# Optimization experiments

Measured on AMD Instinct MI355X. Metric: run time of the kernel, lower is better.

## Reference

```python
import jax, jax.numpy as jnp
import numpy as np

N = 30000; F = 16; E = 300000
HD = 256; NH = 8; C = HD // NH; L = 3
S = 256; K = 128
NH_CA = 4; HDC = HD // NH_CA


def _ln(x, g, b):
    mu = jnp.mean(x, -1, keepdims=True)
    v = jnp.mean((x - mu) ** 2, -1, keepdims=True)
    return (x - mu) / jnp.sqrt(v + 1e-5) * g + b


def setup_inputs() -> dict:
    ks = iter(jax.random.split(jax.random.key(0), 64))
    def nrm(sh, s=0.05):
        return jax.random.normal(next(ks), sh, jnp.float32) * s
    def zeros(sh):
        return jnp.zeros(sh, jnp.float32)
    def ones(sh):
        return jnp.ones(sh, jnp.float32)
    inp = {}
    inp['x'] = jax.random.normal(next(ks), (N, F), jnp.float32)
    inp['edge_index'] = jax.random.randint(next(ks), (2, E), 0, N, jnp.int32)
    inp['batch'] = jnp.zeros((N,), jnp.int32)
    inp['sheet_node_idx'] = jax.random.randint(next(ks), (S, K), 0, N, jnp.int32)
    inp['sheet_features'] = jax.random.normal(next(ks), (S, F), jnp.float32)
    # pre_transform
    inp['pre_W'] = nrm((F, HD)); inp['pre_b'] = zeros((HD,))
    # stacked GATv2 layers (lin_l, lin_r, att, bias)
    inp['gat_Wl'] = nrm((L, HD, HD)); inp['gat_Wr'] = nrm((L, HD, HD))
    inp['gat_att'] = nrm((L, NH, C)); inp['gat_b'] = zeros((L, HD))
    # geometry encoder
    inp['geo_W1'] = nrm((F, HD)); inp['geo_b1'] = zeros((HD,))
    inp['geo_g1'] = ones((HD,)); inp['geo_be1'] = zeros((HD,))
    inp['geo_W2'] = nrm((HD, HD)); inp['geo_b2'] = zeros((HD,))
    inp['geo_g2'] = ones((HD,)); inp['geo_be2'] = zeros((HD,))
    # cross attention (4 heads)
    inp['ca_Wq'] = nrm((HD, HD)); inp['ca_bq'] = zeros((HD,))
    inp['ca_Wk'] = nrm((HD, HD)); inp['ca_bk'] = zeros((HD,))
    inp['ca_Wv'] = nrm((HD, HD)); inp['ca_bv'] = zeros((HD,))
    inp['ca_Wo'] = nrm((HD, HD)); inp['ca_bo'] = zeros((HD,))
    # q_mlp
    inp['q_W1'] = nrm((2 * HD, HD)); inp['q_b1'] = zeros((HD,))
    inp['q_g1'] = ones((HD,)); inp['q_be1'] = zeros((HD,))
    inp['q_W2'] = nrm((HD, HD // 2)); inp['q_b2'] = zeros((HD // 2,))
    inp['q_g2'] = ones((HD // 2,)); inp['q_be2'] = zeros((HD // 2,))
    inp['q_W3'] = nrm((HD // 2, 1)); inp['q_b3'] = zeros((1,))
    # state_done_predictor
    inp['d_W1'] = nrm((HD, HD // 2)); inp['d_b1'] = zeros((HD // 2,))
    inp['d_g1'] = ones((HD // 2,)); inp['d_be1'] = zeros((HD // 2,))
    inp['d_W2'] = nrm((HD // 2, 1)); inp['d_b2'] = zeros((1,))
    return inp


def _fwd(x, sheet_features, pre_W, pre_b, gat_Wl, gat_Wr, gat_att, gat_b,
         geo_W1, geo_b1, geo_g1, geo_be1, geo_W2, geo_b2, geo_g2, geo_be2,
         ca_Wq, ca_bq, ca_Wk, ca_bk, ca_Wv, ca_bv, ca_Wo, ca_bo,
         q_W1, q_b1, q_g1, q_be1, q_W2, q_b2, q_g2, q_be2, q_W3, q_b3,
         d_W1, d_b1, d_g1, d_be1, d_W2, d_b2,
         edge_index, batch, sheet_node_idx):
    loops = jnp.arange(N, dtype=edge_index.dtype)  # PyG GATv2Conv add_self_loops=True
    src = jnp.concatenate([edge_index[0], loops])
    dst = jnp.concatenate([edge_index[1], loops])
    h = x @ pre_W + pre_b  # [N, HD]
    for l in range(L):
        xl = (h @ gat_Wl[l]).reshape(N, NH, C)  # source messages
        xr = (h @ gat_Wr[l]).reshape(N, NH, C)  # target
        m = jax.nn.leaky_relu(xl[src] + xr[dst], 0.2)  # [E+N, NH, C]
        e = jnp.einsum('ehc,hc->eh', m, gat_att[l])
        emax = jax.ops.segment_max(e, dst, num_segments=N)
        a = jnp.exp(e - emax[dst])
        denom = jax.ops.segment_sum(a, dst, num_segments=N)
        alpha = a / (denom[dst] + 1e-16)  # scatter softmax over incoming edges
        h = jax.ops.segment_sum(alpha[:, :, None] * xl[src], dst, num_segments=N)
        h = jax.nn.elu(h.reshape(N, HD) + gat_b[l])
    cnt = jax.ops.segment_sum(jnp.ones((N,), h.dtype), batch, num_segments=1)
    g = jax.ops.segment_sum(h, batch, num_segments=1) / cnt[:, None]  # [1, HD]
    sheet = h[sheet_node_idx].mean(axis=1)  # [S, HD] per-sheet gather+mean
    geo = jax.nn.relu(_ln(sheet_features @ geo_W1 + geo_b1, geo_g1, geo_be1))
    geo = jax.nn.relu(_ln(geo @ geo_W2 + geo_b2, geo_g2, geo_be2))
    qh = (sheet @ ca_Wq + ca_bq).reshape(S, NH_CA, HDC)
    kh = (geo @ ca_Wk + ca_bk).reshape(S, NH_CA, HDC)
    vh = (geo @ ca_Wv + ca_bv).reshape(S, NH_CA, HDC)
    att = jax.nn.softmax(jnp.einsum('qhd,khd->hqk', qh, kh) / jnp.sqrt(jnp.float32(HDC)), axis=-1)
    fused = jnp.einsum('hqk,khd->qhd', att, vh).reshape(S, HD) @ ca_Wo + ca_bo
    hq = jnp.concatenate([fused, jnp.broadcast_to(g, (S, HD))], axis=1)  # [S, 2*HD]
    hq = jax.nn.relu(_ln(hq @ q_W1 + q_b1, q_g1, q_be1))
    hq = jax.nn.relu(_ln(hq @ q_W2 + q_b2, q_g2, q_be2))
    q_values = (hq @ q_W3 + q_b3)[:, 0]  # [S]
    hd = jax.nn.relu(_ln(g @ d_W1 + d_b1, d_g1, d_be1))
    done_logit = (hd @ d_W2 + d_b2)[:, 0]  # [1]
    return q_values, done_logit


def reference(x, edge_index, batch, sheet_node_idx, sheet_features, pre_W, pre_b,
              gat_Wl, gat_Wr, gat_att, gat_b,
              geo_W1, geo_b1, geo_g1, geo_be1, geo_W2, geo_b2, geo_g2, geo_be2,
              ca_Wq, ca_bq, ca_Wk, ca_bk, ca_Wv, ca_bv, ca_Wo, ca_bo,
              q_W1, q_b1, q_g1, q_be1, q_W2, q_b2, q_g2, q_be2, q_W3, q_b3,
              d_W1, d_b1, d_g1, d_be1, d_W2, d_b2):
    return _fwd(x, sheet_features, pre_W, pre_b, gat_Wl, gat_Wr, gat_att, gat_b,
                geo_W1, geo_b1, geo_g1, geo_be1, geo_W2, geo_b2, geo_g2, geo_be2,
                ca_Wq, ca_bq, ca_Wk, ca_bk, ca_Wv, ca_bv, ca_Wo, ca_bo,
                q_W1, q_b1, q_g1, q_be1, q_W2, q_b2, q_g2, q_be2, q_W3, q_b3,
                d_W1, d_b1, d_g1, d_be1, d_W2, d_b2,
                edge_index, batch, sheet_node_idx)
```

## Files before the change

### kernel.cpp

```cpp
#include <hip/hip_runtime.h>
#include <hip/hip_bf16.h>
#include <stdint.h>

#define NN 30000
#define MPAD 30080
#define FI 16
#define EE 300000
#define ETOT (EE + NN)
#define HD 256
#define NH 8
#define CH 32
#define NL 3
#define SS 256
#define KS 128
#define NHC 4
#define HC 64
#define GSB 256
#define RPB 118
#define SCB 118

typedef _Float16 half8 __attribute__((ext_vector_type(8)));
typedef _Float16 half4v __attribute__((ext_vector_type(4)));
typedef _Float16 half2v __attribute__((ext_vector_type(2)));
typedef float f32x4 __attribute__((ext_vector_type(4)));

__device__ __forceinline__ float wsum(float v) {
#pragma unroll
  for (int d = 1; d < 64; d <<= 1) v += __shfl_xor(v, d);
  return v;
}

__device__ __forceinline__ half2v mk2(_Float16 a, _Float16 b) {
  half2v r; r[0] = a; r[1] = b; return r;
}

__device__ __forceinline__ half2v h2max(half2v a, half2v b) {
#if __has_builtin(__builtin_elementwise_max)
  return __builtin_elementwise_max(a, b);
#else
  half2v r; r[0] = a[0] > b[0] ? a[0] : b[0]; r[1] = a[1] > b[1] ? a[1] : b[1];
  return r;
#endif
}

__device__ __forceinline__ float h2dot(half2v a, half2v b, float c) {
#if __has_builtin(__builtin_amdgcn_fdot2)
  return __builtin_amdgcn_fdot2(a, b, c, false);
#else
  return c + (float)a[0] * (float)b[0] + (float)a[1] * (float)b[1];
#endif
}

__device__ __forceinline__ float ln_fast(float a, int t, int n, float* red16,
    const float* __restrict__ G, const float* __restrict__ Be, bool relu)
{
  float av = (t < n) ? a : 0.f;
  float s = wsum(av), s2 = wsum(av * av);
  if ((t & 63) == 0) { red16[t >> 6] = s; red16[8 + (t >> 6)] = s2; }
  __syncthreads();
  float sum = red16[0] + red16[1] + red16[2] + red16[3];
  float sq  = red16[8] + red16[9] + red16[10] + red16[11];
  float mu = sum / n;
  float var = sq / n - mu * mu;
  float o = 0.f;
  if (t < n) {
    o = (a - mu) * rsqrtf(var + 1e-5f) * G[t] + Be[t];
    if (relu) o = fmaxf(o, 0.f);
  }
  __syncthreads();
  return o;
}

__global__ __launch_bounds__(256) void k_init(int* __restrict__ cnt,
    int* __restrict__ gcnt, _Float16* __restrict__ h16pad, int* __restrict__ csr_pad)
{
  int i = blockIdx.x * 256 + threadIdx.x;
  if (i < NN) cnt[i] = 0;
  if (i == 0) gcnt[0] = 0;
  if (i < 8) csr_pad[i] = 0;
  if (i < (MPAD - NN) * HD) h16pad[i] = (_Float16)0.f;
}

__global__ __launch_bounds__(256) void k_wconvAll(
    const float* __restrict__ Wl, const float* __restrict__ Wr,
    const float* __restrict__ geo_W2, const float* __restrict__ ca_Wq,
    const float* __restrict__ ca_Wk, const float* __restrict__ ca_Wv,
    const float* __restrict__ ca_Wo, const float* __restrict__ q_W1,
    const float* __restrict__ q_W2,
    _Float16* __restrict__ WT,
    _Float16* __restrict__ Tgeo2, _Float16* __restrict__ Tq,
    _Float16* __restrict__ Tk, _Float16* __restrict__ Tv,
    _Float16* __restrict__ To, _Float16* __restrict__ Tq1,
    _Float16* __restrict__ Tq2)
{
  int b = blockIdx.x, t = threadIdx.x;
  if (b < 1536) {
    int m = b >> 8;
    int n = b & 255;
    int l = m >> 1;
    const float* W = (m & 1) ? (Wr + (size_t)l * HD * HD) : (Wl + (size_t)l * HD * HD);
    WT[((size_t)m * HD + n) * HD + t] = (_Float16)W[t * HD + n];
    return;
  }
  b -= 1536;
  if (b < 1280) {
    int seg = b >> 8;
    int n = b & 255;
    const float* src = (seg == 0) ? geo_W2 : (seg == 1) ? ca_Wq : (seg == 2) ? ca_Wk
                     : (seg == 3) ? ca_Wv : ca_Wo;
    _Float16* dst = (seg == 0) ? Tgeo2 : (seg == 1) ? Tq : (seg == 2) ? Tk
                  : (seg == 3) ? Tv : To;
    dst[(size_t)n * 256 + t] = (_Float16)src[(size_t)t * 256 + n];
  } else if (b < 1536) {
    int n = b - 1280;
    Tq1[(size_t)n * 512 + t]       = (_Float16)q_W1[(size_t)t * 256 + n];
    Tq1[(size_t)n * 512 + 256 + t] = (_Float16)q_W1[(size_t)(256 + t) * 256 + n];
  } else {
    int n = b - 1536;
    Tq2[(size_t)n * 256 + t] = (_Float16)q_W2[(size_t)t * 128 + n];
  }
}

__global__ __launch_bounds__(256) void k_pre(const float* __restrict__ x,
    const float* __restrict__ W, const float* __restrict__ b,
    _Float16* __restrict__ H16)
{
  __shared__ float Ws[FI][HD];
  __shared__ float xs[8][FI];
  int r0 = blockIdx.x * 8;
  int t = threadIdx.x;
  for (int i = t; i < FI * HD; i += 256) Ws[i >> 8][i & 255] = W[i];
  if (t < 8 * FI) xs[t >> 4][t & 15] = x[(size_t)(r0 + (t >> 4)) * FI + (t & 15)];
  __syncthreads();
  float bj = b[t];
  for (int r = 0; r < 8; ++r) {
    float acc = bj;
#pragma unroll
    for (int k = 0; k < FI; ++k) acc += xs[r][k] * Ws[k][t];
    H16[(size_t)(r0 + r) * HD + t] = (_Float16)acc;
  }
}

__global__ __launch_bounds__(256) void k_count(const int* __restrict__ ei, int* __restrict__ cnt)
{
  int i = blockIdx.x * 256 + threadIdx.x;
  if (i >= ETOT) return;
  int dst = (i < EE) ? ei[EE + i] : (i - EE);
  atomicAdd(&cnt[dst], 1);
}

__global__ __launch_bounds__(256) void k_scanA(const int* __restrict__ cnt,
    int* __restrict__ rowptr, int* __restrict__ btot)
{
  __shared__ int wt[4];
  int b = blockIdx.x, t = threadIdx.x;
  int i = b * 256 + t;
  int v = (i < NN) ? cnt[i] : 0;
  int lane = t & 63, w = t >> 6;
  int s = v;
#pragma unroll
  for (int d = 1; d < 64; d <<= 1) {
    int u = __shfl_up(s, d);
    if (lane >= d) s += u;
  }
  if (lane == 63) wt[w] = s;
  __syncthreads();
  int off = 0;
  for (int k = 0; k < w; ++k) off += wt[k];
  if (i < NN) rowptr[i] = off + s - v;
  if (t == 255) btot[b] = off + s;
}

__global__ __launch_bounds__(128) void k_scanB(const int* __restrict__ btot,
    int* __restrict__ boff, int* __restrict__ rowptr)
{
  __shared__ int wt[2];
  int t = threadIdx.x;
  int v = (t < SCB) ? btot[t] : 0;
  int lane = t & 63, w = t >> 6;
  int s = v;
#pragma unroll
  for (int d = 1; d < 64; d <<= 1) {
    int u = __shfl_up(s, d);
    if (lane >= d) s += u;
  }
  if (lane == 63) wt[w] = s;
  __syncthreads();
  int off = (w == 1) ? wt[0] : 0;
  if (t < SCB) boff[t] = off + s - v;
  if (t == 127) rowptr[NN] = wt[0] + wt[1];
}

__global__ __launch_bounds__(256) void k_scanC(int* __restrict__ rowptr,
    const int* __restrict__ boff, int* __restrict__ wptr)
{
  int b = blockIdx.x, t = threadIdx.x;
  int i = b * 256 + t;
  if (i < NN) {
    int r = rowptr[i] + boff[b];
    rowptr[i] = r;
    wptr[i] = r;
  }
}

__global__ __launch_bounds__(256) void k_scatter(const int* __restrict__ ei,
    int* __restrict__ wptr, int* __restrict__ csr_src)
{
  int i = blockIdx.x * 256 + threadIdx.x;
  if (i >= ETOT) return;
  int src = (i < EE) ? ei[i] : (i - EE);
  int dst = (i < EE) ? ei[EE + i] : (i - EE);
  int pos = atomicAdd(&wptr[dst], 1);
  csr_src[pos] = src;
}

#define BKG 64
__global__ __launch_bounds__(512) void k_gemm16(const _Float16* __restrict__ A,
    const _Float16* __restrict__ WT,
    _Float16* __restrict__ Xl, _Float16* __restrict__ Xr)
{
  __shared__ __align__(16) _Float16 As[128 * BKG];
  __shared__ __align__(16) _Float16 Bs[256 * BKG];
  int t = threadIdx.x;
  int w = t >> 6, lane = t & 63;
  int row0 = blockIdx.x * 128;
  int ct = blockIdx.y;
  const _Float16* Bmat = WT + (size_t)ct * HD * HD;
  _Float16* Out = ct ? Xr : Xl;

  f32x4 acc[4][4] = {};
  int wr = w >> 2, wc = w & 3;

  for (int k0 = 0; k0 < HD; k0 += BKG) {
#pragma unroll
    for (int i = 0; i < 2; ++i) {
      int p = i * 512 + t;
      int row = p >> 3, s = p & 7;
      int g = s ^ (row & 7);
      __builtin_amdgcn_global_load_lds(
        (const __attribute__((address_space(1))) void*)(A + (size_t)(row0 + row) * HD + k0 + g * 8),
        (__attribute__((address_space(3))) void*)((char*)As + (i * 8 + w) * 1024),
        16, 0, 0);
    }
#pragma unroll
    for (int i = 0; i < 4; ++i) {
      int p = i * 512 + t;
      int row = p >> 3, s = p & 7;
      int g = s ^ (row & 7);
      __builtin_amdgcn_global_load_lds(
        (const __attribute__((address_space(1))) void*)(Bmat + (size_t)row * HD + k0 + g * 8),
        (__attribute__((address_space(3))) void*)((char*)Bs + (i * 8 + w) * 1024),
        16, 0, 0);
    }
    __syncthreads();
#pragma unroll
    for (int ks = 0; ks < 2; ++ks) {
      half8 af[4], bfr[4];
      int kslot = ks * 4 + (lane >> 4);
#pragma unroll
      for (int mi = 0; mi < 4; ++mi) {
        int rl = wr * 64 + mi * 16 + (lane & 15);
        int ps = kslot ^ (rl & 7);
        af[mi] = *(const half8*)((const char*)As + rl * 128 + ps * 16);
      }
#pragma unroll
      for (int ni = 0; ni < 4; ++ni) {
        int nl = wc * 64 + ni * 16 + (lane & 15);
        int ps = kslot ^ (nl & 7);
        bfr[ni] = *(const half8*)((const char*)Bs + nl * 128 + ps * 16);
      }
#pragma unroll
      for (int mi = 0; mi < 4; ++mi)
#pragma unroll
        for (int ni = 0; ni < 4; ++ni)
          acc[mi][ni] = __builtin_amdgcn_mfma_f32_16x16x32_f16(af[mi], bfr[ni], acc[mi][ni], 0, 0, 0);
    }
    __syncthreads();
  }
  int crow = (lane >> 4) * 4;
  int ccol = lane & 15;
#pragma unroll
  for (int mi = 0; mi < 4; ++mi)
#pragma unroll
    for (int ni = 0; ni < 4; ++ni) {
      size_t base_r = row0 + wr * 64 + mi * 16 + crow;
      int c = wc * 64 + ni * 16 + ccol;
#pragma unroll
      for (int r = 0; r < 4; ++r)
        Out[(base_r + r) * HD + c] = (_Float16)acc[mi][ni][r];
    }
}

__global__ __launch_bounds__(256) void k_edgeagg(const _Float16* __restrict__ Xl,
    const _Float16* __restrict__ Xr, const float* __restrict__ attw,
    const float* __restrict__ bias, const int* __restrict__ rowptr,
    const int* __restrict__ csr_src, _Float16* __restrict__ H16)
{
  int node = blockIdx.x * 4 + (threadIdx.x >> 6);
  int lane = threadIdx.x & 63;
  if (node >= NN) return;
  int st = rowptr[node], en = rowptr[node + 1];
  int n = en - st;
  int hf = lane >> 5, sl = lane & 31;
  int c = sl * 8;
  half8 xrv = *(const half8*)(Xr + (size_t)node * HD + c);
  float4 wa = *(const float4*)(attw + c);
  float4 wb = *(const float4*)(attw + c + 4);
  half2v w0 = mk2((_Float16)wa.x, (_Float16)wa.y);
  half2v w1 = mk2((_Float16)wa.z, (_Float16)wa.w);
  half2v w2 = mk2((_Float16)wb.x, (_Float16)wb.y);
  half2v w3 = mk2((_Float16)wb.z, (_Float16)wb.w);
  half2v r0 = mk2(xrv[0], xrv[1]), r1 = mk2(xrv[2], xrv[3]);
  half2v r2 = mk2(xrv[4], xrv[5]), r3 = mk2(xrv[6], xrv[7]);
  half2v c02 = mk2((_Float16)0.2f, (_Float16)0.2f);

  float mh = -1e30f, dsum = 0.f;
  half2v acch0 = {}, acch1 = {}, acch2 = {}, acch3 = {};
  int trips = (n + 1) >> 1;
  int base = st + hf;

  half8 b0 = *(const half8*)(Xl + (size_t)csr_src[base] * HD + c);
  half8 b1 = *(const half8*)(Xl + (size_t)csr_src[base + 2] * HD + c);
  half8 b2 = *(const half8*)(Xl + (size_t)csr_src[base + 4] * HD + c);

  for (int it = 0; it < trips; ++it) {
    bool valid = (2 * it + hf) < n;
    half8 xc = b0;
    b0 = b1; b1 = b2;
    {
      int nidx = csr_src[base + 2 * (it + 3)];
      b2 = *(const half8*)(Xl + (size_t)nidx * HD + c);
    }
    half2v x0 = mk2(xc[0], xc[1]), x1 = mk2(xc[2], xc[3]);
    half2v x2 = mk2(xc[4], xc[5]), x3 = mk2(xc[6], xc[7]);
    half2v s0 = x0 + r0, s1 = x1 + r1, s2 = x2 + r2, s3 = x3 + r3;
    half2v m0 = h2max(s0, s0 * c02);
    half2v m1 = h2max(s1, s1 * c02);
    half2v m2 = h2max(s2, s2 * c02);
    half2v m3 = h2max(s3, s3 * c02);
    float eA = h2dot(m1, w1, h2dot(m0, w0, 0.f));
    float eB = h2dot(m3, w3, h2dot(m2, w2, 0.f));
    float e = eA + eB;
    e += __shfl_xor(e, 1);
    e += __shfl_xor(e, 2);
    e = valid ? e : -1e30f;
    if (__any(e > mh + 4.f)) {
      float nm = fmaxf(mh, e);
      float sc = __expf(mh - nm);
      _Float16 sch16 = (_Float16)sc;
      half2v sch = mk2(sch16, sch16);
      acch0 *= sch; acch1 *= sch; acch2 *= sch; acch3 *= sch;
      dsum *= sc;
      mh = nm;
    }
    float pw = valid ? __expf(e - mh) : 0.f;
    _Float16 pwh16 = (_Float16)pw;
    half2v pwh = mk2(pwh16, pwh16);
    acch0 += pwh * x0;
    acch1 += pwh * x1;
    acch2 += pwh * x2;
    acch3 += pwh * x3;
    dsum += pw;
  }
  float a[8];
  a[0] = (float)acch0[0]; a[1] = (float)acch0[1];
  a[2] = (float)acch1[0]; a[3] = (float)acch1[1];
  a[4] = (float)acch2[0]; a[5] = (float)acch2[1];
  a[6] = (float)acch3[0]; a[7] = (float)acch3[1];
  float om = __shfl_xor(mh, 32);
  float od = __shfl_xor(dsum, 32);
  float nm = fmaxf(mh, om);
  float scs = __expf(mh - nm);
  float sco = __expf(om - nm);
  float d = dsum * scs + od * sco;
#pragma unroll
  for (int j = 0; j < 8; ++j) {
    float oa = __shfl_xor(a[j], 32);
    a[j] = a[j] * scs + oa * sco;
  }
  if (hf == 0) {
    float inv = 1.f / (d + 1e-16f);
    float4 ba = *(const float4*)(bias + c);
    float4 bb = *(const float4*)(bias + c + 4);
    float ob[8] = {ba.x, ba.y, ba.z, ba.w, bb.x, bb.y, bb.z, bb.w};
    half8 h8;
#pragma unroll
    for (int j = 0; j < 8; ++j) {
      float o = a[j] * inv + ob[j];
      o = (o > 0.f) ? o : expm1f(o);
      h8[j] = (_Float16)o;
    }
    *(half8*)(H16 + (size_t)node * HD + c) = h8;
  }
}

__global__ __launch_bounds__(256) void k_gsum(const _Float16* __restrict__ H,
    const int* __restrict__ batch, float* __restrict__ gpart, int* __restrict__ gcnt)
{
  __shared__ float flagf[RPB];
  __shared__ int scount;
  int b = blockIdx.x, t = threadIdx.x;
  int r0 = b * RPB;
  int nr = NN - r0; if (nr > RPB) nr = RPB; if (nr < 0) nr = 0;
  if (t == 0) scount = 0;
  __syncthreads();
  if (t < nr) {
    int ok = (batch[r0 + t] == 0) ? 1 : 0;
    flagf[t] = (float)ok;
    if (ok) atomicAdd(&scount, 1);
  }
  __syncthreads();
  float a0 = 0.f, a1 = 0.f, a2 = 0.f, a3 = 0.f;
  const _Float16* Hp = H + (size_t)r0 * HD + t;
  int r = 0;
  for (; r + 4 <= nr; r += 4) {
    float v0 = (float)Hp[(size_t)(r + 0) * HD];
    float v1 = (float)Hp[(size_t)(r + 1) * HD];
    float v2 = (float)Hp[(size_t)(r + 2) * HD];
    float v3 = (float)Hp[(size_t)(r + 3) * HD];
    a0 += v0 * flagf[r + 0]; a1 += v1 * flagf[r + 1];
    a2 += v2 * flagf[r + 2]; a3 += v3 * flagf[r + 3];
  }
  for (; r < nr; ++r) a0 += (float)Hp[(size_t)r * HD] * flagf[r];
  gpart[(size_t)b * HD + t] = (a0 + a1) + (a2 + a3);
  if (t == 0 && scount) atomicAdd(gcnt, scount);
}

__global__ __launch_bounds__(256) void k_tail1(const _Float16* __restrict__ h16,
    const int* __restrict__ sheet_idx, const float* __restrict__ sheet_feat,
    const float* __restrict__ geo_W1, const float* __restrict__ geo_b1,
    const float* __restrict__ geo_g1, const float* __restrict__ geo_be1,
    const float* __restrict__ gpart, const int* __restrict__ gcnt,
    float* __restrict__ gvec,
    _Float16* __restrict__ sh16, _Float16* __restrict__ g116)
{
  __shared__ float xf[FI];
  __shared__ int sidx[KS];
  __shared__ float red16[16];
  int s = blockIdx.x, t = threadIdx.x;

  if (s == SS) {
    float a0 = 0.f, a1 = 0.f, a2 = 0.f, a3 = 0.f;
    for (int b = 0; b < GSB; b += 4) {
      a0 += gpart[(size_t)b * HD + t];
      a1 += gpart[(size_t)(b + 1) * HD + t];
      a2 += gpart[(size_t)(b + 2) * HD + t];
      a3 += gpart[(size_t)(b + 3) * HD + t];
    }
    gvec[t] = ((a0 + a1) + (a2 + a3)) / (float)(*gcnt);
    return;
  }

  if (t < KS) sidx[t] = sheet_idx[s * KS + t];
  if (t >= 240) xf[t - 240] = sheet_feat[s * FI + (t - 240)];
  __syncthreads();

  float pa[8] = {};
#pragma unroll 2
  for (int r = 0; r < KS; r += 8) {
#pragma unroll
    for (int u = 0; u < 8; ++u)
      pa[u] += (float)h16[(size_t)sidx[r + u] * HD + t];
  }
  float shv = ((pa[0] + pa[1]) + (pa[2] + pa[3]) + (pa[4] + pa[5]) + (pa[6] + pa[7])) * (1.f / KS);
  sh16[(size_t)s * HD + t] = (_Float16)shv;

  float a = geo_b1[t];
#pragma unroll
  for (int k = 0; k < FI; ++k) a += xf[k] * geo_W1[k * HD + t];
  float g1 = ln_fast(a, t, 256, red16, geo_g1, geo_be1, true);
  g116[(size_t)s * HD + t] = (_Float16)g1;
}

template <int KD, int NW>
__global__ __launch_bounds__(NW * 64) void k_stageLN(
    const _Float16* __restrict__ X, const _Float16* __restrict__ WT,
    const float* __restrict__ b, const float* __restrict__ G,
    const float* __restrict__ Be, _Float16* __restrict__ Y,
    const float* __restrict__ W3, const float* __restrict__ b3,
    float* __restrict__ outq,
    const float* __restrict__ gvec,
    const float* __restrict__ dW1, const float* __restrict__ db1,
    const float* __restrict__ dg1, const float* __restrict__ dbe1,
    const float* __restrict__ dW2, const float* __restrict__ db2,
    float* __restrict__ outd)
{
  __shared__ float ps[NW * 16], ps2[NW * 16], pq[NW * 16];
  const int NCOL = NW * 64;
  int t = threadIdx.x;

  if (outd != nullptr && blockIdx.x == 16) {
    int w2 = t >> 6;
    float acc2 = db1[t];
    for (int k = 0; k < 256; ++k) acc2 += gvec[k] * dW1[(size_t)k * 128 + t];
    float s = wsum(acc2), s2v = wsum(acc2 * acc2);
    if ((t & 63) == 0) { ps[w2] = s; ps2[w2] = s2v; }
    __syncthreads();
    float S = ps[0] + ps[1], S2 = ps2[0] + ps2[1];
    float mu = S * (1.f / 128.f), var = S2 * (1.f / 128.f) - mu * mu;
    float hdv = fmaxf((acc2 - mu) * rsqrtf(var + 1e-5f) * dg1[t] + dbe1[t], 0.f);
    float o = wsum(hdv * dW2[t]);
    if ((t & 63) == 0) pq[w2] = o;
    __syncthreads();
    if (t == 0) outd[0] = pq[0] + pq[1] + db2[0];
    return;
  }

  int w = t >> 6, lane = t & 63;
  int arow = lane & 15, kg = lane >> 4;
  int m0 = blockIdx.x * 16;
  int col0 = w * 64;

  f32x4 acc[4] = {};
#pragma unroll
  for (int ks = 0; ks < KD / 32; ++ks) {
    half8 af = *(const half8*)(X + (size_t)(m0 + arow) * KD + ks * 32 + kg * 8);
#pragma unroll
    for (int n = 0; n < 4; ++n) {
      half8 bf = *(const half8*)(WT + (size_t)(col0 + n * 16 + arow) * KD + ks * 32 + kg * 8);
      acc[n] = __builtin_amdgcn_mfma_f32_16x16x32_f16(af, bf, acc[n], 0, 0, 0);
    }
  }
#pragma unroll
  for (int n = 0; n < 4; ++n) {
    float bv = b[col0 + n * 16 + arow];
#pragma unroll
    for (int r = 0; r < 4; ++r) acc[n][r] += bv;
  }
  float s[4] = {}, s2[4] = {};
#pragma unroll
  for (int n = 0; n < 4; ++n)
#pragma unroll
    for (int r = 0; r < 4; ++r) { float v = acc[n][r]; s[r] += v; s2[r] += v * v; }
#pragma unroll
  for (int d = 1; d < 16; d <<= 1)
#pragma unroll
    for (int r = 0; r < 4; ++r) { s[r] += __shfl_xor(s[r], d); s2[r] += __shfl_xor(s2[r], d); }
  if (arow == 0) {
#pragma unroll
    for (int r = 0; r < 4; ++r) {
      ps[w * 16 + kg * 4 + r] = s[r];
      ps2[w * 16 + kg * 4 + r] = s2[r];
    }
  }
  __syncthreads();
  float mu[4], rs[4];
#pragma unroll
  for (int r = 0; r < 4; ++r) {
    float S = 0.f, S2 = 0.f;
#pragma unroll
    for (int w2 = 0; w2 < NW; ++w2) { S += ps[w2 * 16 + kg * 4 + r]; S2 += ps2[w2 * 16 + kg * 4 + r]; }
    float m = S / NCOL;
    float var = S2 / NCOL - m * m;
    mu[r] = m; rs[r] = rsqrtf(var + 1e-5f);
  }
#pragma unroll
  for (int n = 0; n < 4; ++n) {
    int col = col0 + n * 16 + arow;
    float gv = G[col], bev = Be[col];
#pragma unroll
    for (int r = 0; r < 4; ++r)
      acc[n][r] = fmaxf((acc[n][r] - mu[r]) * rs[r] * gv + bev, 0.f);
  }
  if (Y) {
#pragma unroll
    for (int n = 0; n < 4; ++n) {
      int col = col0 + n * 16 + arow;
#pragma unroll
      for (int r = 0; r < 4; ++r)
        Y[(size_t)(m0 + kg * 4 + r) * NCOL + col] = (_Float16)acc[n][r];
    }
  }
  if (outq) {
    float p[4] = {};
#pragma unroll
    for (int n = 0; n < 4; ++n) {
      float w3 = W3[col0 + n * 16 + arow];
#pragma unroll
      for (int r = 0; r < 4; ++r) p[r] += acc[n][r] * w3;
    }
#pragma unroll
    for (int d = 1; d < 16; d <<= 1)
#pragma unroll
      for (int r = 0; r < 4; ++r) p[r] += __shfl_xor(p[r], d);
    if (arow == 0)
#pragma unroll
      for (int r = 0; r < 4; ++r) pq[w * 16 + kg * 4 + r] = p[r];
    __syncthreads();
    if (w == 0 && arow == 0) {
#pragma unroll
      for (int r = 0; r < 4; ++r) {
        float o = b3[0];
#pragma unroll
        for (int w2 = 0; w2 < NW; ++w2) o += pq[w2 * 16 + kg * 4 + r];
        outq[m0 + kg * 4 + r] = o;
      }
    }
  }
}

__global__ __launch_bounds__(64) void k_qkv(
    const _Float16* __restrict__ sh16, const _Float16* __restrict__ g216,
    const _Float16* __restrict__ Tq, const _Float16* __restrict__ Tk,
    const _Float16* __restrict__ Tv,
    const float* __restrict__ bq, const float* __restrict__ bk,
    const float* __restrict__ bv,
    _Float16* __restrict__ qb, _Float16* __restrict__ kb, _Float16* __restrict__ vb)
{
  int lane = threadIdx.x;
  int arow = lane & 15, kg = lane >> 4;
  int m0 = blockIdx.x * 16;
  int col0 = blockIdx.y * 64;
  int mat = blockIdx.z;
  const _Float16* X = (mat == 0) ? sh16 : g216;
  const _Float16* WT = (mat == 0) ? Tq : (mat == 1) ? Tk : Tv;
  const float* b = (mat == 0) ? bq : (mat == 1) ? bk : bv;
  _Float16* Y = (mat == 0) ? qb : (mat == 1) ? kb : vb;

  f32x4 acc[4] = {};
#pragma unroll
  for (int ks = 0; ks < 8; ++ks) {
    half8 af = *(const half8*)(X + (size_t)(m0 + arow) * 256 + ks * 32 + kg * 8);
#pragma unroll
    for (int n = 0; n < 4; ++n) {
      half8 bf = *(const half8*)(WT + (size_t)(col0 + n * 16 + arow) * 256 + ks * 32 + kg * 8);
      acc[n] = __builtin_amdgcn_mfma_f32_16x16x32_f16(af, bf, acc[n], 0, 0, 0);
    }
  }
#pragma unroll
  for (int n = 0; n < 4; ++n) {
    int col = col0 + n * 16 + arow;
    float bv2 = b[col];
#pragma unroll
    for (int r = 0; r < 4; ++r)
      Y[(size_t)(m0 + kg * 4 + r) * 256 + col] = (_Float16)(acc[n][r] + bv2);
  }
}

__global__ __launch_bounds__(64) void k_wo(
    const _Float16* __restrict__ pv16, const _Float16* __restrict__ To,
    const float* __restrict__ bo, const float* __restrict__ gvec,
    _Float16* __restrict__ hqin)
{
  int lane = threadIdx.x;
  int arow = lane & 15, kg = lane >> 4;
  int m0 = blockIdx.x * 16;
  int col0 = blockIdx.y * 64;

  f32x4 acc[4] = {};
#pragma unroll
  for (int ks = 0; ks < 8; ++ks) {
    half8 af = *(const half8*)(pv16 + (size_t)(m0 + arow) * 256 + ks * 32 + kg * 8);
#pragma unroll
    for (int n = 0; n < 4; ++n) {
      half8 bf = *(const half8*)(To + (size_t)(col0 + n * 16 + arow) * 256 + ks * 32 + kg * 8);
      acc[n] = __builtin_amdgcn_mfma_f32_16x16x32_f16(af, bf, acc[n], 0, 0, 0);
    }
  }
#pragma unroll
  for (int n = 0; n < 4; ++n) {
    int col = col0 + n * 16 + arow;
    float bv = bo[col];
    _Float16 gg = (_Float16)gvec[col];
#pragma unroll
    for (int r = 0; r < 4; ++r) {
      hqin[(size_t)(m0 + kg * 4 + r) * 512 + col] = (_Float16)(acc[n][r] + bv);
      hqin[(size_t)(m0 + kg * 4 + r) * 512 + 256 + col] = gg;
    }
  }
}

__global__ __launch_bounds__(1024) void k_attn(const _Float16* __restrict__ qb,
    const _Float16* __restrict__ kb, const _Float16* __restrict__ vb,
    _Float16* __restrict__ pv16)
{
  __shared__ float qv[HD];
  __shared__ float att[1024];
  __shared__ float red4[1024];
  __shared__ float redm[16];
  __shared__ float reds[16];
  int row = blockIdx.x, t = threadIdx.x;
  int w = t >> 6;

  if (t < 256) qv[t] = (float)qb[(size_t)row * HD + t];
  __syncthreads();

  int h = t >> 8, key = t & 255;
  float e = 0.f;
  {
    const half8* kr = (const half8*)(kb + (size_t)key * HD + h * HC);
    const float* qh = qv + h * HC;
#pragma unroll
    for (int d = 0; d < 8; ++d) {
      half8 kk = kr[d];
#pragma unroll
      for (int u = 0; u < 8; ++u) e += qh[d * 8 + u] * (float)kk[u];
    }
    e *= 0.125f;
  }
  float wm = e;
#pragma unroll
  for (int d = 1; d < 64; d <<= 1) wm = fmaxf(wm, __shfl_xor(wm, d));
  if ((t & 63) == 0) redm[w] = wm;
  __syncthreads();
  float mx = fmaxf(fmaxf(redm[4 * h], redm[4 * h + 1]), fmaxf(redm[4 * h + 2], redm[4 * h + 3]));
  float pw = __expf(e - mx);
  float ws = wsum(pw);
  if ((t & 63) == 0) reds[w] = ws;
  att[t] = pw;
  __syncthreads();

  int kq = t >> 8, j = t & 255;
  int hj = j >> 6;
  float p = 0.f;
  const float* arow = att + hj * 256 + kq * 64;
  const _Float16* vcol = vb + (size_t)(kq * 64) * HD + j;
  for (int k = 0; k < 64; ++k)
    p += arow[k] * (float)vcol[(size_t)k * HD];
  red4[t] = p;
  __syncthreads();
  if (t < 256) {
    int hh = t >> 6;
    float dsum = reds[4 * hh] + reds[4 * hh + 1] + reds[4 * hh + 2] + reds[4 * hh + 3];
    float pv = (red4[t] + red4[256 + t] + red4[512 + t] + red4[768 + t]) / dsum;
    pv16[(size_t)row * HD + t] = (_Float16)pv;
  }
}

extern "C" void kernel_launch(void* const* d_in, const int* in_sizes, int n_in,
                              void* d_out, int out_size, void* d_ws, size_t ws_size,
                              hipStream_t stream) {
  const float* x      = (const float*)d_in[0];
  const int*   ei     = (const int*)d_in[1];
  const int*   batch  = (const int*)d_in[2];
  const int*   sheet_idx = (const int*)d_in[3];
  const float* sheet_feat = (const float*)d_in[4];
  const float* pre_W  = (const float*)d_in[5];
  const float* pre_b  = (const float*)d_in[6];
  const float* gat_Wl = (const float*)d_in[7];
  const float* gat_Wr = (const float*)d_in[8];
  const float* gat_att = (const float*)d_in[9];
  const float* gat_b  = (const float*)d_in[10];
  const float* geo_W1 = (const float*)d_in[11];
  const float* geo_b1 = (const float*)d_in[12];
  const float* geo_g1 = (const float*)d_in[13];
  const float* geo_be1 = (const float*)d_in[14];
  const float* geo_W2 = (const float*)d_in[15];
  const float* geo_b2 = (const float*)d_in[16];
  const float* geo_g2 = (const float*)d_in[17];
  const float* geo_be2 = (const float*)d_in[18];
  const float* ca_Wq = (const float*)d_in[19];
  const float* ca_bq = (const float*)d_in[20];
  const float* ca_Wk = (const float*)d_in[21];
  const float* ca_bk = (const float*)d_in[22];
  const float* ca_Wv = (const float*)d_in[23];
  const float* ca_bv = (const float*)d_in[24];
  const float* ca_Wo = (const float*)d_in[25];
  const float* ca_bo = (const float*)d_in[26];
  const float* q_W1 = (const float*)d_in[27];
  const float* q_b1 = (const float*)d_in[28];
  const float* q_g1 = (const float*)d_in[29];
  const float* q_be1 = (const float*)d_in[30];
  const float* q_W2 = (const float*)d_in[31];
  const float* q_b2 = (const float*)d_in[32];
  const float* q_g2 = (const float*)d_in[33];
  const float* q_be2 = (const float*)d_in[34];
  const float* q_W3 = (const float*)d_in[35];
  const float* q_b3 = (const float*)d_in[36];
  const float* d_W1 = (const float*)d_in[37];
  const float* d_b1 = (const float*)d_in[38];
  const float* d_g1 = (const float*)d_in[39];
  const float* d_be1 = (const float*)d_in[40];
  const float* d_W2 = (const float*)d_in[41];
  const float* d_b2 = (const float*)d_in[42];

  char* wsb = (char*)d_ws;
  auto alloc = [&](size_t bytes) { char* p = wsb; wsb += (bytes + 255) & ~(size_t)255; return p; };

  _Float16* h16  = (_Float16*)alloc((size_t)MPAD * HD * 2);
  _Float16* Xl16 = (_Float16*)alloc((size_t)MPAD * HD * 2);
  _Float16* Xr16 = (_Float16*)alloc((size_t)MPAD * HD * 2);
  _Float16* WT   = (_Float16*)alloc((size_t)6 * HD * HD * 2);
  _Float16* Tgeo2 = (_Float16*)alloc((size_t)HD * HD * 2);
  _Float16* Tq   = (_Float16*)alloc((size_t)HD * HD * 2);
  _Float16* Tk   = (_Float16*)alloc((size_t)HD * HD * 2);
  _Float16* Tv   = (_Float16*)alloc((size_t)HD * HD * 2);
  _Float16* To   = (_Float16*)alloc((size_t)HD * HD * 2);
  _Float16* Tq1  = (_Float16*)alloc((size_t)HD * 512 * 2);
  _Float16* Tq2  = (_Float16*)alloc((size_t)128 * HD * 2);
  _Float16* sh16 = (_Float16*)alloc((size_t)SS * HD * 2);
  _Float16* g116 = (_Float16*)alloc((size_t)SS * HD * 2);
  _Float16* g216 = (_Float16*)alloc((size_t)SS * HD * 2);
  _Float16* qb16 = (_Float16*)alloc((size_t)SS * HD * 2);
  _Float16* kb16 = (_Float16*)alloc((size_t)SS * HD * 2);
  _Float16* vb16 = (_Float16*)alloc((size_t)SS * HD * 2);
  _Float16* pv16 = (_Float16*)alloc((size_t)SS * HD * 2);
  _Float16* hqin16 = (_Float16*)alloc((size_t)SS * 512 * 2);
  _Float16* hq116 = (_Float16*)alloc((size_t)SS * HD * 2);
  float* gpart   = (float*)alloc((size_t)GSB * HD * 4);
  float* gvec    = (float*)alloc(256 * 4);
  int* cnt       = (int*)alloc((size_t)NN * 4);
  int* rowptr    = (int*)alloc((size_t)(NN + 1) * 4);
  int* wptr      = (int*)alloc((size_t)NN * 4);
  int* csr_src   = (int*)alloc((size_t)(ETOT + 8) * 4);
  int* btot      = (int*)alloc((size_t)SCB * 4);
  int* boff      = (int*)alloc((size_t)SCB * 4);
  int* gcnt      = (int*)alloc(4);

  float* out_q = (float*)d_out;
  float* out_d = out_q + SS;

  k_init<<<118, 256, 0, stream>>>(cnt, gcnt, h16 + (size_t)NN * HD, csr_src + ETOT);

  k_count<<<(ETOT + 255) / 256, 256, 0, stream>>>(ei, cnt);
  k_scanA<<<SCB, 256, 0, stream>>>(cnt, rowptr, btot);
  k_scanB<<<1, 128, 0, stream>>>(btot, boff, rowptr);
  k_scanC<<<SCB, 256, 0, stream>>>(rowptr, boff, wptr);
  k_scatter<<<(ETOT + 255) / 256, 256, 0, stream>>>(ei, wptr, csr_src);

  k_wconvAll<<<3200, 256, 0, stream>>>(gat_Wl, gat_Wr, geo_W2, ca_Wq, ca_Wk, ca_Wv,
                                       ca_Wo, q_W1, q_W2,
                                       WT, Tgeo2, Tq, Tk, Tv, To, Tq1, Tq2);
  k_pre<<<NN / 8, 256, 0, stream>>>(x, pre_W, pre_b, h16);

  dim3 ggrid(MPAD / 128, 2);
  for (int l = 0; l < NL; ++l) {
    k_gemm16<<<ggrid, 512, 0, stream>>>(h16, WT + (size_t)l * 2 * HD * HD, Xl16, Xr16);
    k_edgeagg<<<(NN + 3) / 4, 256, 0, stream>>>(Xl16, Xr16, gat_att + l * NH * CH,
                                                gat_b + l * HD, rowptr, csr_src, h16);
  }

  k_gsum<<<GSB, 256, 0, stream>>>(h16, batch, gpart, gcnt);

  k_tail1<<<SS + 1, 256, 0, stream>>>(h16, sheet_idx, sheet_feat,
      geo_W1, geo_b1, geo_g1, geo_be1, gpart, gcnt, gvec, sh16, g116);
  k_stageLN<256, 4><<<16, 256, 0, stream>>>(g116, Tgeo2, geo_b2, geo_g2, geo_be2,
      g216, nullptr, nullptr, nullptr,
      nullptr, nullptr, nullptr, nullptr, nullptr, nullptr, nullptr, nullptr);
  dim3 qkvg(16, 4, 3);
  k_qkv<<<qkvg, 64, 0, stream>>>(sh16, g216, Tq, Tk, Tv, ca_bq, ca_bk, ca_bv,
                                 qb16, kb16, vb16);
  k_attn<<<SS, 1024, 0, stream>>>(qb16, kb16, vb16, pv16);
  dim3 wog(16, 4);
  k_wo<<<wog, 64, 0, stream>>>(pv16, To, ca_bo, gvec, hqin16);
  k_stageLN<512, 4><<<16, 256, 0, stream>>>(hqin16, Tq1, q_b1, q_g1, q_be1,
      hq116, nullptr, nullptr, nullptr,
      nullptr, nullptr, nullptr, nullptr, nullptr, nullptr, nullptr, nullptr);
  k_stageLN<256, 2><<<17, 128, 0, stream>>>(hq116, Tq2, q_b2, q_g2, q_be2,
      nullptr, q_W3, q_b3, out_q,
      gvec, d_W1, d_b1, d_g1, d_be1, d_W2, d_b2, out_d);
}
```

Measured before the change: 303.4 us.

## Fuse init into weight conversion, restructure GAT GEMM tiling, prescale CSR indices

Measured after the change: 286.1 us. 5.7% less time.

```diff
diff --git a/kernel.cpp b/kernel.cpp
--- a/kernel.cpp
+++ b/kernel.cpp
@@ -71,16 +71,6 @@
   return o;
 }
 
-__global__ __launch_bounds__(256) void k_init(int* __restrict__ cnt,
-    int* __restrict__ gcnt, _Float16* __restrict__ h16pad, int* __restrict__ csr_pad)
-{
-  int i = blockIdx.x * 256 + threadIdx.x;
-  if (i < NN) cnt[i] = 0;
-  if (i == 0) gcnt[0] = 0;
-  if (i < 8) csr_pad[i] = 0;
-  if (i < (MPAD - NN) * HD) h16pad[i] = (_Float16)0.f;
-}
-
 __global__ __launch_bounds__(256) void k_wconvAll(
     const float* __restrict__ Wl, const float* __restrict__ Wr,
     const float* __restrict__ geo_W2, const float* __restrict__ ca_Wq,
@@ -91,9 +81,19 @@
     _Float16* __restrict__ Tgeo2, _Float16* __restrict__ Tq,
     _Float16* __restrict__ Tk, _Float16* __restrict__ Tv,
     _Float16* __restrict__ To, _Float16* __restrict__ Tq1,
-    _Float16* __restrict__ Tq2)
+    _Float16* __restrict__ Tq2,
+    int* __restrict__ cnt, int* __restrict__ gcnt,
+    _Float16* __restrict__ h16pad, int* __restrict__ csr_pad)
 {
   int b = blockIdx.x, t = threadIdx.x;
+  if (b >= 3200) {
+    int i = (b - 3200) * 256 + t;
+    if (i < NN) cnt[i] = 0;
+    if (i == 0) gcnt[0] = 0;
+    if (i < 8) csr_pad[i] = 0;
+    if (i < (MPAD - NN) * HD) h16pad[i] = (_Float16)0.f;
+    return;
+  }
   if (b < 1536) {
     int m = b >> 8;
     int n = b & 255;
@@ -211,7 +211,7 @@
   int src = (i < EE) ? ei[i] : (i - EE);
   int dst = (i < EE) ? ei[EE + i] : (i - EE);
   int pos = atomicAdd(&wptr[dst], 1);
-  csr_src[pos] = src;
+  csr_src[pos] = src * HD;
 }
 
 #define BKG 64
@@ -219,36 +219,30 @@
     const _Float16* __restrict__ WT,
     _Float16* __restrict__ Xl, _Float16* __restrict__ Xr)
 {
-  __shared__ __align__(16) _Float16 As[128 * BKG];
-  __shared__ __align__(16) _Float16 Bs[256 * BKG];
+  __shared__ __align__(16) _Float16 As[64 * BKG];
+  __shared__ __align__(16) _Float16 Bs[512 * BKG];
   int t = threadIdx.x;
   int w = t >> 6, lane = t & 63;
-  int row0 = blockIdx.x * 128;
-  int ct = blockIdx.y;
-  const _Float16* Bmat = WT + (size_t)ct * HD * HD;
-  _Float16* Out = ct ? Xr : Xl;
+  int row0 = blockIdx.x * 64;
 
   f32x4 acc[4][4] = {};
-  int wr = w >> 2, wc = w & 3;
 
   for (int k0 = 0; k0 < HD; k0 += BKG) {
-#pragma unroll
-    for (int i = 0; i < 2; ++i) {
+    {
+      int row = t >> 3, s = t & 7;
+      int g = s ^ (row & 7);
+      __builtin_amdgcn_global_load_lds(
+        (const __attribute__((address_space(1))) void*)(A + (size_t)(row0 + row) * HD + k0 + g * 8),
+        (__attribute__((address_space(3))) void*)((char*)As + w * 1024),
+        16, 0, 0);
+    }
+#pragma unroll
+    for (int i = 0; i < 8; ++i) {
       int p = i * 512 + t;
       int row = p >> 3, s = p & 7;
       int g = s ^ (row & 7);
       __builtin_amdgcn_global_load_lds(
-        (const __attribute__((address_space(1))) void*)(A + (size_t)(row0 + row) * HD + k0 + g * 8),
-        (__attribute__((address_space(3))) void*)((char*)As + (i * 8 + w) * 1024),
-        16, 0, 0);
-    }
-#pragma unroll
-    for (int i = 0; i < 4; ++i) {
-      int p = i * 512 + t;
-      int row = p >> 3, s = p & 7;
-      int g = s ^ (row & 7);
-      __builtin_amdgcn_global_load_lds(
-        (const __attribute__((address_space(1))) void*)(Bmat + (size_t)row * HD + k0 + g * 8),
+        (const __attribute__((address_space(1))) void*)(WT + (size_t)row * HD + k0 + g * 8),
         (__attribute__((address_space(3))) void*)((char*)Bs + (i * 8 + w) * 1024),
         16, 0, 0);
     }
@@ -259,13 +253,13 @@
       int kslot = ks * 4 + (lane >> 4);
 #pragma unroll
       for (int mi = 0; mi < 4; ++mi) {
-        int rl = wr * 64 + mi * 16 + (lane & 15);
+        int rl = mi * 16 + (lane & 15);
         int ps = kslot ^ (rl & 7);
         af[mi] = *(const half8*)((const char*)As + rl * 128 + ps * 16);
       }
 #pragma unroll
       for (int ni = 0; ni < 4; ++ni) {
-        int nl = wc * 64 + ni * 16 + (lane & 15);
+        int nl = w * 64 + ni * 16 + (lane & 15);
         int ps = kslot ^ (nl & 7);
         bfr[ni] = *(const half8*)((const char*)Bs + nl * 128 + ps * 16);
       }
@@ -279,12 +273,14 @@
   }
   int crow = (lane >> 4) * 4;
   int ccol = lane & 15;
+  _Float16* Out = (w < 4) ? Xl : Xr;
+  int cbase = (w < 4) ? (w * 64) : ((w - 4) * 64);
 #pragma unroll
   for (int mi = 0; mi < 4; ++mi)
 #pragma unroll
     for (int ni = 0; ni < 4; ++ni) {
-      size_t base_r = row0 + wr * 64 + mi * 16 + crow;
-      int c = wc * 64 + ni * 16 + ccol;
+      size_t base_r = row0 + mi * 16 + crow;
+      int c = cbase + ni * 16 + ccol;
 #pragma unroll
       for (int r = 0; r < 4; ++r)
         Out[(base_r + r) * HD + c] = (_Float16)acc[mi][ni][r];
@@ -319,17 +315,17 @@
   int trips = (n + 1) >> 1;
   int base = st + hf;
 
-  half8 b0 = *(const half8*)(Xl + (size_t)csr_src[base] * HD + c);
-  half8 b1 = *(const half8*)(Xl + (size_t)csr_src[base + 2] * HD + c);
-  half8 b2 = *(const half8*)(Xl + (size_t)csr_src[base + 4] * HD + c);
+  half8 b0 = *(const half8*)(Xl + (size_t)csr_src[base] + c);
+  half8 b1 = *(const half8*)(Xl + (size_t)csr_src[base + 2] + c);
+  half8 b2 = *(const half8*)(Xl + (size_t)csr_src[base + 4] + c);
 
   for (int it = 0; it < trips; ++it) {
     bool valid = (2 * it + hf) < n;
     half8 xc = b0;
     b0 = b1; b1 = b2;
     {
-      int nidx = csr_src[base + 2 * (it + 3)];
-      b2 = *(const half8*)(Xl + (size_t)nidx * HD + c);
+      int noff = csr_src[base + 2 * (it + 3)];
+      b2 = *(const half8*)(Xl + (size_t)noff + c);
     }
     half2v x0 = mk2(xc[0], xc[1]), x1 = mk2(xc[2], xc[3]);
     half2v x2 = mk2(xc[4], xc[5]), x3 = mk2(xc[6], xc[7]);
@@ -387,7 +383,7 @@
 #pragma unroll
     for (int j = 0; j < 8; ++j) {
       float o = a[j] * inv + ob[j];
-      o = (o > 0.f) ? o : expm1f(o);
+      o = (o > 0.f) ? o : (__expf(o) - 1.f);
       h8[j] = (_Float16)o;
     }
     *(half8*)(H16 + (size_t)node * HD + c) = h8;
@@ -810,7 +806,10 @@
   float* out_q = (float*)d_out;
   float* out_d = out_q + SS;
 
-  k_init<<<118, 256, 0, stream>>>(cnt, gcnt, h16 + (size_t)NN * HD, csr_src + ETOT);
+  k_wconvAll<<<3318, 256, 0, stream>>>(gat_Wl, gat_Wr, geo_W2, ca_Wq, ca_Wk, ca_Wv,
+                                       ca_Wo, q_W1, q_W2,
+                                       WT, Tgeo2, Tq, Tk, Tv, To, Tq1, Tq2,
+                                       cnt, gcnt, h16 + (size_t)NN * HD, csr_src + ETOT);
 
   k_count<<<(ETOT + 255) / 256, 256, 0, stream>>>(ei, cnt);
   k_scanA<<<SCB, 256, 0, stream>>>(cnt, rowptr, btot);
@@ -818,14 +817,10 @@
   k_scanC<<<SCB, 256, 0, stream>>>(rowptr, boff, wptr);
   k_scatter<<<(ETOT + 255) / 256, 256, 0, stream>>>(ei, wptr, csr_src);
 
-  k_wconvAll<<<3200, 256, 0, stream>>>(gat_Wl, gat_Wr, geo_W2, ca_Wq, ca_Wk, ca_Wv,
-                                       ca_Wo, q_W1, q_W2,
-                                       WT, Tgeo2, Tq, Tk, Tv, To, Tq1, Tq2);
   k_pre<<<NN / 8, 256, 0, stream>>>(x, pre_W, pre_b, h16);
 
-  dim3 ggrid(MPAD / 128, 2);
   for (int l = 0; l < NL; ++l) {
-    k_gemm16<<<ggrid, 512, 0, stream>>>(h16, WT + (size_t)l * 2 * HD * HD, Xl16, Xr16);
+    k_gemm16<<<MPAD / 64, 512, 0, stream>>>(h16, WT + (size_t)l * 2 * HD * HD, Xl16, Xr16);
     k_edgeagg<<<(NN + 3) / 4, 256, 0, stream>>>(Xl16, Xr16, gat_att + l * NH * CH,
                                                 gat_b + l * HD, rowptr, csr_src, h16);
   }
```
